# Optimization experiments

Measured on AMD Instinct MI355X. Metric: run time of the kernel, lower is better.

The kernel has to match this reference:

```python
import jax, jax.numpy as jnp
import numpy as np

H = 16       # num_attention_heads
D = 64       # head_dim
WIN = 256    # local attention window_size


def setup_inputs() -> dict:
    key = jax.random.key(0)
    ks = jax.random.split(key, 6)
    B, S, E = 2, 2048, 1024
    sc = 1.0 / np.sqrt(E)
    return {
        "hidden_states": jax.random.normal(ks[0], (B, S, E), jnp.float32),
        "Wq": jax.random.normal(ks[1], (E, E), jnp.float32) * sc,
        "Wk": jax.random.normal(ks[2], (E, E), jnp.float32) * sc,
        "Wv": jax.random.normal(ks[3], (E, E), jnp.float32) * sc,
        "Wo": jax.random.normal(ks[4], (E, E), jnp.float32) * sc,
        "bo": jnp.zeros((E,), jnp.float32),
    }


def reference(hidden_states, Wq, Wk, Wv, Wo, bo):
    B, S, E = hidden_states.shape
    # torch Linear: y = x @ W^T
    q = (hidden_states @ Wq.T).reshape(B, S, H, D).transpose(0, 2, 1, 3)  # [B,H,S,D]
    k = (hidden_states @ Wk.T).reshape(B, S, H, D).transpose(0, 2, 1, 3)
    v = (hidden_states @ Wv.T).reshape(B, S, H, D).transpose(0, 2, 1, 3)

    # Eager path: fp32 QK^T, NO 1/sqrt(d) scaling (faithful to source)
    scores = jnp.einsum("bhqd,bhkd->bhqk", q.astype(jnp.float32), k.astype(jnp.float32))

    i = jnp.arange(S)[:, None]
    j = jnp.arange(S)[None, :]
    band = (j <= i) & (j > i - WIN)  # [S,S]
    mask_value = jnp.finfo(scores.dtype).min
    scores = jnp.where(band[None, None], scores, mask_value)

    attn = jax.nn.softmax(scores, axis=-1).astype(v.dtype)  # dropout p=0 -> identity
    ctx = jnp.einsum("bhqk,bhkd->bhqd", attn, v)              # [B,H,S,D]
    ctx = ctx.transpose(0, 2, 1, 3).reshape(B, S, E)          # merge heads
    return ctx @ Wo.T + bo
```

## Files before the change

### kernel.cpp

```cpp
#include <hip/hip_runtime.h>


typedef __bf16 bf16x8 __attribute__((ext_vector_type(8)));
typedef short s16x8 __attribute__((ext_vector_type(8)));
typedef float f32x4 __attribute__((ext_vector_type(4)));
typedef unsigned short u16;

#define DEV __device__ __forceinline__

DEV u16 f2bf(float f) {
  unsigned u = __builtin_bit_cast(unsigned, f);
  u += 0x7FFFu + ((u >> 16) & 1u);
  return (u16)(u >> 16);
}
DEV float bf2f(u16 h) {
  unsigned u = ((unsigned)h) << 16;
  return __builtin_bit_cast(float, u);
}

#define MFMA16(a, b, c) __builtin_amdgcn_mfma_f32_16x16x32_bf16((a), (b), (c), 0, 0, 0)

template <bool LO>
__global__ __launch_bounds__(256) void cvt_split(const float* __restrict__ src,
                                                 u16* __restrict__ hi,
                                                 u16* __restrict__ lo, int n4) {
  for (int i = blockIdx.x * 256 + threadIdx.x; i < n4; i += gridDim.x * 256) {
    f32x4 v = ((const f32x4*)src)[i];
    unsigned long long ph = 0, pl = 0;
#pragma unroll
    for (int c = 0; c < 4; ++c) {
      u16 h = f2bf(v[c]);
      ph |= ((unsigned long long)h) << (16 * c);
      if (LO) {
        u16 l = f2bf(v[c] - bf2f(h));
        pl |= ((unsigned long long)l) << (16 * c);
      }
    }
    ((unsigned long long*)hi)[i] = ph;
    if (LO) ((unsigned long long*)lo)[i] = pl;
  }
}

template <int MODE>
__global__ __launch_bounds__(256) void gemm_kernel(
    const u16* __restrict__ Ah, const u16* __restrict__ Al,
    const u16* __restrict__ Bh, const u16* __restrict__ Bl,
    u16* __restrict__ O1, u16* __restrict__ O2,
    const float* __restrict__ bias, float* __restrict__ Of) {
  constexpr bool SPLIT = (MODE == 0);
  constexpr int NS = SPLIT ? 2 : 1;
  constexpr int BKP = 40;
  __shared__ u16 sA[NS][128][BKP];
  __shared__ u16 sB[NS][128][BKP];

  const int tid = threadIdx.x;
  const int lane = tid & 63, w = tid >> 6;
  const int lr = lane & 15, lg = lane >> 4;
  const int wr = w >> 1, wc = w & 1;
  const int m0 = blockIdx.y * 128, n0 = blockIdx.x * 128;

  f32x4 acc[4][4];
#pragma unroll
  for (int i = 0; i < 4; ++i)
#pragma unroll
    for (int j = 0; j < 4; ++j)
#pragma unroll
      for (int e = 0; e < 4; ++e) acc[i][j][e] = 0.f;

  for (int k0 = 0; k0 < 1024; k0 += 32) {
#pragma unroll
    for (int c = 0; c < 2; ++c) {
      int cid = c * 256 + tid;
      int row = cid >> 2, col8 = (cid & 3) * 8;
      size_t aoff = (size_t)(m0 + row) * 1024 + k0 + col8;
      size_t boff = (size_t)(n0 + row) * 1024 + k0 + col8;
      *(s16x8*)&sA[0][row][col8] = *(const s16x8*)&Ah[aoff];
      *(s16x8*)&sB[0][row][col8] = *(const s16x8*)&Bh[boff];
      if constexpr (SPLIT) {
        *(s16x8*)&sA[1][row][col8] = *(const s16x8*)&Al[aoff];
        *(s16x8*)&sB[1][row][col8] = *(const s16x8*)&Bl[boff];
      }
    }
    __syncthreads();

    bf16x8 fah[4], fbh[4], fal[4], fbl[4];
#pragma unroll
    for (int f = 0; f < 4; ++f) {
      fah[f] = *(const bf16x8*)&sA[0][wr * 64 + f * 16 + lr][lg * 8];
      fbh[f] = *(const bf16x8*)&sB[0][wc * 64 + f * 16 + lr][lg * 8];
      if constexpr (SPLIT) {
        fal[f] = *(const bf16x8*)&sA[1][wr * 64 + f * 16 + lr][lg * 8];
        fbl[f] = *(const bf16x8*)&sB[1][wc * 64 + f * 16 + lr][lg * 8];
      }
    }
#pragma unroll
    for (int i = 0; i < 4; ++i)
#pragma unroll
      for (int j = 0; j < 4; ++j) {
        acc[i][j] = MFMA16(fah[i], fbh[j], acc[i][j]);
        if constexpr (SPLIT) {
          acc[i][j] = MFMA16(fah[i], fbl[j], acc[i][j]);
          acc[i][j] = MFMA16(fal[i], fbh[j], acc[i][j]);
        }
      }
    __syncthreads();
  }

#pragma unroll
  for (int i = 0; i < 4; ++i)
#pragma unroll
    for (int j = 0; j < 4; ++j)
#pragma unroll
      for (int e = 0; e < 4; ++e) {
        float v = acc[i][j][e];
        int mm = m0 + wr * 64 + i * 16 + lg * 4 + e;
        int nn = n0 + wc * 64 + j * 16 + lr;
        if constexpr (MODE == 0) {
          int bb = mm >> 11, ss = mm & 2047, hh = nn >> 6, dd = nn & 63;
          size_t idx = ((size_t)(bb * 16 + hh) * 2048 + ss) * 64 + dd;
          u16 h = f2bf(v);
          O1[idx] = h;
          O2[idx] = f2bf(v - bf2f(h));
        } else if constexpr (MODE == 1) {
          int bb = mm >> 11, ss = mm & 2047, hh = nn >> 6, dd = nn & 63;
          size_t idx = ((size_t)(bb * 16 + hh) * 64 + dd) * 2048 + ss;
          O1[idx] = f2bf(v);
        } else {
          Of[(size_t)mm * 1024 + nn] = v + bias[nn];
        }
      }
}

__global__ __launch_bounds__(256) void attn_kernel(
    const u16* __restrict__ qh, const u16* __restrict__ ql,
    const u16* __restrict__ kh, const u16* __restrict__ kl,
    const u16* __restrict__ vT, u16* __restrict__ ctx) {
  const int qt = blockIdx.x, hd = blockIdx.y, b = blockIdx.z;
  const int q0 = qt * 64;
  const int bh = b * 16 + hd;
  const int tid = threadIdx.x;
  const int lane = tid & 63, w = tid >> 6;
  const int lr = lane & 15, lg = lane >> 4;

  __shared__ u16 sKh[64][72];
  __shared__ u16 sKl[64][72];
  __shared__ u16 sVT[64][72];
  __shared__ u16 sP[4][16][72];

  bf16x8 qfh[2], qfl[2];
  const size_t qbase = ((size_t)bh * 2048 + q0 + w * 16 + lr) * 64;
#pragma unroll
  for (int ks = 0; ks < 2; ++ks) {
    qfh[ks] = *(const bf16x8*)&qh[qbase + ks * 32 + lg * 8];
    qfl[ks] = *(const bf16x8*)&ql[qbase + ks * 32 + lg * 8];
  }

  float mrow[4], lrow[4];
  f32x4 cf[4];
#pragma unroll
  for (int e = 0; e < 4; ++e) { mrow[e] = -__builtin_inff(); lrow[e] = 0.f; }
#pragma unroll
  for (int nd = 0; nd < 4; ++nd)
#pragma unroll
    for (int e = 0; e < 4; ++e) cf[nd][e] = 0.f;

  const int t0 = (qt >= 4) ? qt - 4 : 0;
  for (int t = t0; t <= qt; ++t) {
    const int k0 = t * 64;
#pragma unroll
    for (int c = 0; c < 2; ++c) {
      int cid = c * 256 + tid;
      int row = cid >> 3, col8 = (cid & 7) * 8;
      size_t kidx = ((size_t)bh * 2048 + k0 + row) * 64 + col8;
      size_t vidx = ((size_t)bh * 64 + row) * 2048 + k0 + col8;
      *(s16x8*)&sKh[row][col8] = *(const s16x8*)&kh[kidx];
      *(s16x8*)&sKl[row][col8] = *(const s16x8*)&kl[kidx];
      *(s16x8*)&sVT[row][col8] = *(const s16x8*)&vT[vidx];
    }
    __syncthreads();

    f32x4 sc[4];
#pragma unroll
    for (int nf = 0; nf < 4; ++nf)
#pragma unroll
      for (int e = 0; e < 4; ++e) sc[nf][e] = 0.f;
#pragma unroll
    for (int ks = 0; ks < 2; ++ks)
#pragma unroll
      for (int nf = 0; nf < 4; ++nf) {
        bf16x8 kbh = *(const bf16x8*)&sKh[nf * 16 + lr][ks * 32 + lg * 8];
        bf16x8 kbl = *(const bf16x8*)&sKl[nf * 16 + lr][ks * 32 + lg * 8];
        sc[nf] = MFMA16(qfh[ks], kbh, sc[nf]);
        sc[nf] = MFMA16(qfh[ks], kbl, sc[nf]);
        sc[nf] = MFMA16(qfl[ks], kbh, sc[nf]);
      }

    const bool masked = (k0 < q0 - 192) || (k0 >= q0);
    if (masked) {
#pragma unroll
      for (int nf = 0; nf < 4; ++nf) {
        int key = k0 + nf * 16 + lr;
#pragma unroll
        for (int e = 0; e < 4; ++e) {
          int qi = q0 + w * 16 + lg * 4 + e;
          if (key > qi || key + 256 <= qi) sc[nf][e] = -__builtin_inff();
        }
      }
    }

    float rm[4];
#pragma unroll
    for (int e = 0; e < 4; ++e)
      rm[e] = fmaxf(fmaxf(sc[0][e], sc[1][e]), fmaxf(sc[2][e], sc[3][e]));
#pragma unroll
    for (int off = 1; off < 16; off <<= 1)
#pragma unroll
      for (int e = 0; e < 4; ++e) rm[e] = fmaxf(rm[e], __shfl_xor(rm[e], off));

    float alpha[4], mu[4];
#pragma unroll
    for (int e = 0; e < 4; ++e) {
      float mn = fmaxf(mrow[e], rm[e]);
      bool ninf = (mn == -__builtin_inff());
      mu[e] = ninf ? 0.f : mn;
      alpha[e] = ninf ? 1.f : __expf(mrow[e] - mn);
      mrow[e] = mn;
    }
    float p[4][4], rs[4];
#pragma unroll
    for (int nf = 0; nf < 4; ++nf)
#pragma unroll
      for (int e = 0; e < 4; ++e) p[nf][e] = __expf(sc[nf][e] - mu[e]);
#pragma unroll
    for (int e = 0; e < 4; ++e) rs[e] = p[0][e] + p[1][e] + p[2][e] + p[3][e];
#pragma unroll
    for (int off = 1; off < 16; off <<= 1)
#pragma unroll
      for (int e = 0; e < 4; ++e) rs[e] += __shfl_xor(rs[e], off);
#pragma unroll
    for (int e = 0; e < 4; ++e) lrow[e] = lrow[e] * alpha[e] + rs[e];
#pragma unroll
    for (int nd = 0; nd < 4; ++nd)
#pragma unroll
      for (int e = 0; e < 4; ++e) cf[nd][e] *= alpha[e];

#pragma unroll
    for (int nf = 0; nf < 4; ++nf)
#pragma unroll
      for (int e = 0; e < 4; ++e)
        sP[w][lg * 4 + e][nf * 16 + lr] = f2bf(p[nf][e]);

#pragma unroll
    for (int ks = 0; ks < 2; ++ks) {
      bf16x8 pa = *(const bf16x8*)&sP[w][lr][ks * 32 + lg * 8];
#pragma unroll
      for (int nd = 0; nd < 4; ++nd) {
        bf16x8 vb = *(const bf16x8*)&sVT[nd * 16 + lr][ks * 32 + lg * 8];
        cf[nd] = MFMA16(pa, vb, cf[nd]);
      }
    }
    __syncthreads();
  }

#pragma unroll
  for (int nd = 0; nd < 4; ++nd)
#pragma unroll
    for (int e = 0; e < 4; ++e) {
      float v = cf[nd][e] / lrow[e];
      size_t o = ((size_t)(b * 2048 + q0 + w * 16 + lg * 4 + e)) * 1024 +
                 hd * 64 + nd * 16 + lr;
      ctx[o] = f2bf(v);
    }
}

extern "C" void kernel_launch(void* const* d_in, const int* in_sizes, int n_in,
                              void* d_out, int out_size, void* d_ws, size_t ws_size,
                              hipStream_t stream) {
  (void)in_sizes; (void)n_in; (void)out_size; (void)ws_size;
  const float* x  = (const float*)d_in[0];
  const float* Wq = (const float*)d_in[1];
  const float* Wk = (const float*)d_in[2];
  const float* Wv = (const float*)d_in[3];
  const float* Wo = (const float*)d_in[4];
  const float* bo = (const float*)d_in[5];
  float* out = (float*)d_out;
  char* ws = (char*)d_ws;

  constexpr size_t TEN = 8388608;
  constexpr size_t WTEN = 2097152;
  u16* xh  = (u16*)(ws + 0 * TEN);
  u16* xl  = (u16*)(ws + 1 * TEN);
  u16* qh  = (u16*)(ws + 2 * TEN);
  u16* ql  = (u16*)(ws + 3 * TEN);
  u16* kh  = (u16*)(ws + 4 * TEN);
  u16* kl  = (u16*)(ws + 5 * TEN);
  u16* vT  = (u16*)(ws + 6 * TEN);
  u16* ctx = (u16*)(ws + 7 * TEN);
  char* wb = ws + 8 * TEN;
  u16* wqh = (u16*)(wb + 0 * WTEN);
  u16* wql = (u16*)(wb + 1 * WTEN);
  u16* wkh = (u16*)(wb + 2 * WTEN);
  u16* wkl = (u16*)(wb + 3 * WTEN);
  u16* wvh = (u16*)(wb + 4 * WTEN);
  u16* woh = (u16*)(wb + 5 * WTEN);

  cvt_split<true><<<1024, 256, 0, stream>>>(x, xh, xl, 4194304 / 4);
  cvt_split<true><<<256, 256, 0, stream>>>(Wq, wqh, wql, 1048576 / 4);
  cvt_split<true><<<256, 256, 0, stream>>>(Wk, wkh, wkl, 1048576 / 4);
  cvt_split<false><<<256, 256, 0, stream>>>(Wv, wvh, nullptr, 1048576 / 4);
  cvt_split<false><<<256, 256, 0, stream>>>(Wo, woh, nullptr, 1048576 / 4);

  dim3 gg(8, 32), bb(256);
  gemm_kernel<0><<<gg, bb, 0, stream>>>(xh, xl, wqh, wql, qh, ql, nullptr, nullptr);
  gemm_kernel<0><<<gg, bb, 0, stream>>>(xh, xl, wkh, wkl, kh, kl, nullptr, nullptr);
  gemm_kernel<1><<<gg, bb, 0, stream>>>(xh, nullptr, wvh, nullptr, vT, nullptr, nullptr, nullptr);
  attn_kernel<<<dim3(32, 16, 2), bb, 0, stream>>>(qh, ql, kh, kl, vT, ctx);
  gemm_kernel<2><<<gg, bb, 0, stream>>>(ctx, nullptr, woh, nullptr, nullptr, nullptr, bo, out);
}
```

Baseline: 280.4 us.

## Fuse conversions and QKV projections into single launches with direct-to-LDS loads

Merges the five fp32-to-bf16 conversion launches into one kernel and the three Q/K/V projection GEMMs into one grid of 24x32 blocks, where each block picks its hi/lo split mode and output layout from its column region. Tile staging now uses global_load_lds so data goes straight from global memory into LDS instead of through registers, and the LDS tile padding is removed. The aim is to cut launch overhead, fill the GPU better with a single larger grid, and reduce register pressure during staging. The unpadded LDS layout may cause bank conflicts on fragment reads, and the runtime branch on region adds some divergence-free control overhead.

Measured after the change: 309.1 us. +10.2%, slower.

```diff
diff --git a/kernel.cpp b/kernel.cpp
--- a/kernel.cpp
+++ b/kernel.cpp
@@ -5,6 +5,7 @@
 typedef short s16x8 __attribute__((ext_vector_type(8)));
 typedef float f32x4 __attribute__((ext_vector_type(4)));
 typedef unsigned short u16;
+typedef unsigned long long u64;
 
 #define DEV __device__ __forceinline__
 
@@ -20,44 +21,71 @@
 
 #define MFMA16(a, b, c) __builtin_amdgcn_mfma_f32_16x16x32_bf16((a), (b), (c), 0, 0, 0)
 
-template <bool LO>
-__global__ __launch_bounds__(256) void cvt_split(const float* __restrict__ src,
-                                                 u16* __restrict__ hi,
-                                                 u16* __restrict__ lo, int n4) {
-  for (int i = blockIdx.x * 256 + threadIdx.x; i < n4; i += gridDim.x * 256) {
-    f32x4 v = ((const f32x4*)src)[i];
-    unsigned long long ph = 0, pl = 0;
+DEV void gload16(const u16* g, u16* l) {
+  __builtin_amdgcn_global_load_lds(
+      (const __attribute__((address_space(1))) void*)(const void*)g,
+      (__attribute__((address_space(3))) void*)(void*)l, 16, 0, 0);
+}
+
+DEV void stage_tile(const u16* __restrict__ g, size_t stride, int r0, int k0,
+                    u16* lds, int w, int lane) {
+#pragma unroll
+  for (int c = 0; c < 2; ++c) {
+    int ch = c * 256 + (w << 6) + lane;
+    gload16(&g[(size_t)(r0 + (ch >> 2)) * stride + k0 + ((ch & 3) << 3)],
+            lds + (size_t)(c * 4 + w) * 512);
+  }
+}
+
+__global__ __launch_bounds__(256) void cvt_all(
+    const float* __restrict__ x, const float* __restrict__ Wq,
+    const float* __restrict__ Wk, const float* __restrict__ Wv,
+    const float* __restrict__ Wo, u16* __restrict__ xh, u16* __restrict__ xl,
+    u16* __restrict__ wh, u16* __restrict__ wl, u16* __restrict__ woh) {
+  for (int i = blockIdx.x * 256 + threadIdx.x; i < 2097152;
+       i += gridDim.x * 256) {
+    const float* src;
+    u16 *dh, *dl = nullptr;
+    int off;
+    bool sp;
+    if (i < 1048576) {
+      src = x; off = i; dh = xh; dl = xl; sp = true;
+    } else {
+      int j = i - 1048576;
+      int r = j >> 18;
+      off = j & 262143;
+      if (r == 0)      { src = Wq; dh = wh;           dl = wl;           sp = true; }
+      else if (r == 1) { src = Wk; dh = wh + 1048576; dl = wl + 1048576; sp = true; }
+      else if (r == 2) { src = Wv; dh = wh + 2097152; sp = false; }
+      else             { src = Wo; dh = woh;          sp = false; }
+    }
+    f32x4 v = ((const f32x4*)src)[off];
+    u64 ph = 0, pl = 0;
 #pragma unroll
     for (int c = 0; c < 4; ++c) {
       u16 h = f2bf(v[c]);
-      ph |= ((unsigned long long)h) << (16 * c);
-      if (LO) {
-        u16 l = f2bf(v[c] - bf2f(h));
-        pl |= ((unsigned long long)l) << (16 * c);
-      }
-    }
-    ((unsigned long long*)hi)[i] = ph;
-    if (LO) ((unsigned long long*)lo)[i] = pl;
-  }
-}
-
-template <int MODE>
-__global__ __launch_bounds__(256) void gemm_kernel(
-    const u16* __restrict__ Ah, const u16* __restrict__ Al,
-    const u16* __restrict__ Bh, const u16* __restrict__ Bl,
-    u16* __restrict__ O1, u16* __restrict__ O2,
-    const float* __restrict__ bias, float* __restrict__ Of) {
-  constexpr bool SPLIT = (MODE == 0);
-  constexpr int NS = SPLIT ? 2 : 1;
-  constexpr int BKP = 40;
-  __shared__ u16 sA[NS][128][BKP];
-  __shared__ u16 sB[NS][128][BKP];
-
-  const int tid = threadIdx.x;
-  const int lane = tid & 63, w = tid >> 6;
+      ph |= ((u64)h) << (16 * c);
+      u16 l = f2bf(v[c] - bf2f(h));
+      pl |= ((u64)l) << (16 * c);
+    }
+    ((u64*)dh)[off] = ph;
+    if (sp) ((u64*)dl)[off] = pl;
+  }
+}
+
+__global__ __launch_bounds__(256, 3) void qkv_gemm(
+    const u16* __restrict__ Xh, const u16* __restrict__ Xl,
+    const u16* __restrict__ Wh, const u16* __restrict__ Wl,
+    u16* __restrict__ qh, u16* __restrict__ ql, u16* __restrict__ kh,
+    u16* __restrict__ kl, u16* __restrict__ vT) {
+  __shared__ u16 sAh[128 * 32], sAl[128 * 32];
+  __shared__ u16 sBh[128 * 32], sBl[128 * 32];
+  const int tid = threadIdx.x, lane = tid & 63, w = tid >> 6;
   const int lr = lane & 15, lg = lane >> 4;
   const int wr = w >> 1, wc = w & 1;
   const int m0 = blockIdx.y * 128, n0 = blockIdx.x * 128;
+  const int region = n0 >> 10;
+  const bool split = region < 2;
 
   f32x4 acc[4][4];
 #pragma unroll
@@ -68,41 +96,41 @@
       for (int e = 0; e < 4; ++e) acc[i][j][e] = 0.f;
 
   for (int k0 = 0; k0 < 1024; k0 += 32) {
-#pragma unroll
-    for (int c = 0; c < 2; ++c) {
-      int cid = c * 256 + tid;
-      int row = cid >> 2, col8 = (cid & 3) * 8;
-      size_t aoff = (size_t)(m0 + row) * 1024 + k0 + col8;
-      size_t boff = (size_t)(n0 + row) * 1024 + k0 + col8;
-      *(s16x8*)&sA[0][row][col8] = *(const s16x8*)&Ah[aoff];
-      *(s16x8*)&sB[0][row][col8] = *(const s16x8*)&Bh[boff];
-      if constexpr (SPLIT) {
-        *(s16x8*)&sA[1][row][col8] = *(const s16x8*)&Al[aoff];
-        *(s16x8*)&sB[1][row][col8] = *(const s16x8*)&Bl[boff];
-      }
+    stage_tile(Xh, 1024, m0, k0, sAh, w, lane);
+    stage_tile(Wh, 1024, n0, k0, sBh, w, lane);
+    if (split) {
+      stage_tile(Xl, 1024, m0, k0, sAl, w, lane);
+      stage_tile(Wl, 1024, n0, k0, sBl, w, lane);
     }
     __syncthreads();
 
     bf16x8 fah[4], fbh[4], fal[4], fbl[4];
 #pragma unroll
     for (int f = 0; f < 4; ++f) {
-      fah[f] = *(const bf16x8*)&sA[0][wr * 64 + f * 16 + lr][lg * 8];
-      fbh[f] = *(const bf16x8*)&sB[0][wc * 64 + f * 16 + lr][lg * 8];
-      if constexpr (SPLIT) {
-        fal[f] = *(const bf16x8*)&sA[1][wr * 64 + f * 16 + lr][lg * 8];
-        fbl[f] = *(const bf16x8*)&sB[1][wc * 64 + f * 16 + lr][lg * 8];
-      }
-    }
-#pragma unroll
-    for (int i = 0; i < 4; ++i)
-#pragma unroll
-      for (int j = 0; j < 4; ++j) {
-        acc[i][j] = MFMA16(fah[i], fbh[j], acc[i][j]);
-        if constexpr (SPLIT) {
+      fah[f] = *(const bf16x8*)&sAh[(wr * 64 + f * 16 + lr) * 32 + lg * 8];
+      fbh[f] = *(const bf16x8*)&sBh[(wc * 64 + f * 16 + lr) * 32 + lg * 8];
+    }
+    if (split) {
+#pragma unroll
+      for (int f = 0; f < 4; ++f) {
+        fal[f] = *(const bf16x8*)&sAl[(wr * 64 + f * 16 + lr) * 32 + lg * 8];
+        fbl[f] = *(const bf16x8*)&sBl[(wc * 64 + f * 16 + lr) * 32 + lg * 8];
+      }
+#pragma unroll
+      for (int i = 0; i < 4; ++i)
+#pragma unroll
+        for (int j = 0; j < 4; ++j) {
+          acc[i][j] = MFMA16(fah[i], fbh[j], acc[i][j]);
           acc[i][j] = MFMA16(fah[i], fbl[j], acc[i][j]);
           acc[i][j] = MFMA16(fal[i], fbh[j], acc[i][j]);
         }
-      }
+    } else {
+#pragma unroll
+      for (int i = 0; i < 4; ++i)
+#pragma unroll
+        for (int j = 0; j < 4; ++j)
+          acc[i][j] = MFMA16(fah[i], fbh[j], acc[i][j]);
+    }
     __syncthreads();
   }
 
@@ -114,20 +142,67 @@
       for (int e = 0; e < 4; ++e) {
         float v = acc[i][j][e];
         int mm = m0 + wr * 64 + i * 16 + lg * 4 + e;
-        int nn = n0 + wc * 64 + j * 16 + lr;
-        if constexpr (MODE == 0) {
-          int bb = mm >> 11, ss = mm & 2047, hh = nn >> 6, dd = nn & 63;
+        int nl = (n0 & 1023) + wc * 64 + j * 16 + lr;
+        int bb = mm >> 11, ss = mm & 2047, hh = nl >> 6, dd = nl & 63;
+        if (region == 0) {
           size_t idx = ((size_t)(bb * 16 + hh) * 2048 + ss) * 64 + dd;
           u16 h = f2bf(v);
-          O1[idx] = h;
-          O2[idx] = f2bf(v - bf2f(h));
-        } else if constexpr (MODE == 1) {
-          int bb = mm >> 11, ss = mm & 2047, hh = nn >> 6, dd = nn & 63;
-          size_t idx = ((size_t)(bb * 16 + hh) * 64 + dd) * 2048 + ss;
-          O1[idx] = f2bf(v);
+          qh[idx] = h;
+          ql[idx] = f2bf(v - bf2f(h));
+        } else if (region == 1) {
+          size_t idx = ((size_t)(bb * 16 + hh) * 2048 + ss) * 64 + dd;
+          u16 h = f2bf(v);
+          kh[idx] = h;
+          kl[idx] = f2bf(v - bf2f(h));
         } else {
-          Of[(size_t)mm * 1024 + nn] = v + bias[nn];
+          vT[((size_t)(bb * 16 + hh) * 64 + dd) * 2048 + ss] = f2bf(v);
         }
+      }
+}
+
+__global__ __launch_bounds__(256) void out_gemm(const u16* __restrict__ ctx,
+                                                const u16* __restrict__ Wo,
+                                                const float* __restrict__ bias,
+                                                float* __restrict__ Of) {
+  __shared__ u16 sA[128 * 32], sB[128 * 32];
+  const int tid = threadIdx.x, lane = tid & 63, w = tid >> 6;
+  const int lr = lane & 15, lg = lane >> 4;
+  const int wr = w >> 1, wc = w & 1;
+  const int m0 = blockIdx.y * 128, n0 = blockIdx.x * 128;
+
+  f32x4 acc[4][4];
+#pragma unroll
+  for (int i = 0; i < 4; ++i)
+#pragma unroll
+    for (int j = 0; j < 4; ++j)
+#pragma unroll
+      for (int e = 0; e < 4; ++e) acc[i][j][e] = 0.f;
+
+  for (int k0 = 0; k0 < 1024; k0 += 32) {
+    stage_tile(ctx, 1024, m0, k0, sA, w, lane);
+    stage_tile(Wo, 1024, n0, k0, sB, w, lane);
+    __syncthreads();
+    bf16x8 fa[4], fb[4];
+#pragma unroll
+    for (int f = 0; f < 4; ++f) {
+      fa[f] = *(const bf16x8*)&sA[(wr * 64 + f * 16 + lr) * 32 + lg * 8];
+      fb[f] = *(const bf16x8*)&sB[(wc * 64 + f * 16 + lr) * 32 + lg * 8];
+    }
+#pragma unroll
+    for (int i = 0; i < 4; ++i)
+#pragma unroll
+      for (int j = 0; j < 4; ++j) acc[i][j] = MFMA16(fa[i], fb[j], acc[i][j]);
+    __syncthreads();
+  }
+#pragma unroll
+  for (int i = 0; i < 4; ++i)
+#pragma unroll
+    for (int j = 0; j < 4; ++j)
+#pragma unroll
+      for (int e = 0; e < 4; ++e) {
+        int mm = m0 + wr * 64 + i * 16 + lg * 4 + e;
+        int nn = n0 + wc * 64 + j * 16 + lr;
+        Of[(size_t)mm * 1024 + nn] = acc[i][j][e] + bias[nn];
       }
 }
 
@@ -286,34 +361,21 @@
   float* out = (float*)d_out;
   char* ws = (char*)d_ws;
 
-  constexpr size_t TEN = 8388608;
-  constexpr size_t WTEN = 2097152;
-  u16* xh  = (u16*)(ws + 0 * TEN);
-  u16* xl  = (u16*)(ws + 1 * TEN);
-  u16* qh  = (u16*)(ws + 2 * TEN);
-  u16* ql  = (u16*)(ws + 3 * TEN);
-  u16* kh  = (u16*)(ws + 4 * TEN);
-  u16* kl  = (u16*)(ws + 5 * TEN);
-  u16* vT  = (u16*)(ws + 6 * TEN);
-  u16* ctx = (u16*)(ws + 7 * TEN);
-  char* wb = ws + 8 * TEN;
-  u16* wqh = (u16*)(wb + 0 * WTEN);
-  u16* wql = (u16*)(wb + 1 * WTEN);
-  u16* wkh = (u16*)(wb + 2 * WTEN);
-  u16* wkl = (u16*)(wb + 3 * WTEN);
-  u16* wvh = (u16*)(wb + 4 * WTEN);
-  u16* woh = (u16*)(wb + 5 * WTEN);
-
-  cvt_split<true><<<1024, 256, 0, stream>>>(x, xh, xl, 4194304 / 4);
-  cvt_split<true><<<256, 256, 0, stream>>>(Wq, wqh, wql, 1048576 / 4);
-  cvt_split<true><<<256, 256, 0, stream>>>(Wk, wkh, wkl, 1048576 / 4);
-  cvt_split<false><<<256, 256, 0, stream>>>(Wv, wvh, nullptr, 1048576 / 4);
-  cvt_split<false><<<256, 256, 0, stream>>>(Wo, woh, nullptr, 1048576 / 4);
-
-  dim3 gg(8, 32), bb(256);
-  gemm_kernel<0><<<gg, bb, 0, stream>>>(xh, xl, wqh, wql, qh, ql, nullptr, nullptr);
-  gemm_kernel<0><<<gg, bb, 0, stream>>>(xh, xl, wkh, wkl, kh, kl, nullptr, nullptr);
-  gemm_kernel<1><<<gg, bb, 0, stream>>>(xh, nullptr, wvh, nullptr, vT, nullptr, nullptr, nullptr);
-  attn_kernel<<<dim3(32, 16, 2), bb, 0, stream>>>(qh, ql, kh, kl, vT, ctx);
-  gemm_kernel<2><<<gg, bb, 0, stream>>>(ctx, nullptr, woh, nullptr, nullptr, nullptr, bo, out);
-}
+  constexpr size_t MB = 1048576;
+  u16* xh  = (u16*)(ws + 0 * MB);
+  u16* xl  = (u16*)(ws + 8 * MB);
+  u16* qh  = (u16*)(ws + 16 * MB);
+  u16* ql  = (u16*)(ws + 24 * MB);
+  u16* kh  = (u16*)(ws + 32 * MB);
+  u16* kl  = (u16*)(ws + 40 * MB);
+  u16* vT  = (u16*)(ws + 48 * MB);
+  u16* ctx = (u16*)(ws + 56 * MB);
+  u16* wh  = (u16*)(ws + 64 * MB);
+  u16* wl  = (u16*)(ws + 70 * MB);
+  u16* woh = (u16*)(ws + 74 * MB);
+
+  cvt_all<<<2048, 256, 0, stream>>>(x, Wq, Wk, Wv, Wo, xh, xl, wh, wl, woh);
+  qkv_gemm<<<dim3(24, 32), 256, 0, stream>>>(xh, xl, wh, wl, qh, ql, kh, kl, vT);
+  attn_kernel<<<dim3(32, 16, 2), 256, 0, stream>>>(qh, ql, kh, kl, vT, ctx);
+  out_gemm<<<dim3(8, 32), 256, 0, stream>>>(ctx, woh, bo, out);
+}
```

## Fuse conversion kernels and store V row-major, transposing in attention LDS

Applied to the files above, without the earlier changes.

Replaces five separate fp32-to-bf16 split conversion launches with one combined kernel covering x and all four weights, which cuts launch overhead. The V projection now writes V in [B,H,S,D] layout instead of a transposed [B,H,D,S] layout, so the GEMM epilogue writes contiguous d indices. The attention kernel then transposes V into shared memory with scalar strided LDS stores, which may cause bank conflicts. The unified conversion loop also computes the low part for every element, even where it is not stored.

New measurement: 276.3 us. Within noise of the previous version (-1.5%).

```diff
diff --git a/kernel.cpp b/kernel.cpp
--- a/kernel.cpp
+++ b/kernel.cpp
@@ -5,6 +5,7 @@
 typedef short s16x8 __attribute__((ext_vector_type(8)));
 typedef float f32x4 __attribute__((ext_vector_type(4)));
 typedef unsigned short u16;
+typedef unsigned long long u64;
 
 #define DEV __device__ __forceinline__
 
@@ -20,24 +21,39 @@
 
 #define MFMA16(a, b, c) __builtin_amdgcn_mfma_f32_16x16x32_bf16((a), (b), (c), 0, 0, 0)
 
-template <bool LO>
-__global__ __launch_bounds__(256) void cvt_split(const float* __restrict__ src,
-                                                 u16* __restrict__ hi,
-                                                 u16* __restrict__ lo, int n4) {
-  for (int i = blockIdx.x * 256 + threadIdx.x; i < n4; i += gridDim.x * 256) {
-    f32x4 v = ((const f32x4*)src)[i];
-    unsigned long long ph = 0, pl = 0;
+__global__ __launch_bounds__(256) void cvt_all(
+    const float* __restrict__ x, const float* __restrict__ Wq,
+    const float* __restrict__ Wk, const float* __restrict__ Wv,
+    const float* __restrict__ Wo, u16* __restrict__ xh, u16* __restrict__ xl,
+    u16* __restrict__ wh, u16* __restrict__ wl, u16* __restrict__ woh) {
+  for (int i = blockIdx.x * 256 + threadIdx.x; i < 2097152;
+       i += gridDim.x * 256) {
+    const float* src;
+    u16 *dh, *dl = nullptr;
+    int off;
+    bool sp;
+    if (i < 1048576) {
+      src = x; off = i; dh = xh; dl = xl; sp = true;
+    } else {
+      int j = i - 1048576;
+      int r = j >> 18;
+      off = j & 262143;
+      if (r == 0)      { src = Wq; dh = wh;           dl = wl;           sp = true; }
+      else if (r == 1) { src = Wk; dh = wh + 1048576; dl = wl + 1048576; sp = true; }
+      else if (r == 2) { src = Wv; dh = wh + 2097152; sp = false; }
+      else             { src = Wo; dh = woh;          sp = false; }
+    }
+    f32x4 v = ((const f32x4*)src)[off];
+    u64 ph = 0, pl = 0;
 #pragma unroll
     for (int c = 0; c < 4; ++c) {
       u16 h = f2bf(v[c]);
-      ph |= ((unsigned long long)h) << (16 * c);
-      if (LO) {
-        u16 l = f2bf(v[c] - bf2f(h));
-        pl |= ((unsigned long long)l) << (16 * c);
-      }
-    }
-    ((unsigned long long*)hi)[i] = ph;
-    if (LO) ((unsigned long long*)lo)[i] = pl;
+      ph |= ((u64)h) << (16 * c);
+      u16 l = f2bf(v[c] - bf2f(h));
+      pl |= ((u64)l) << (16 * c);
+    }
+    ((u64*)dh)[off] = ph;
+    if (sp) ((u64*)dl)[off] = pl;
   }
 }
 
@@ -123,7 +139,7 @@
           O2[idx] = f2bf(v - bf2f(h));
         } else if constexpr (MODE == 1) {
           int bb = mm >> 11, ss = mm & 2047, hh = nn >> 6, dd = nn & 63;
-          size_t idx = ((size_t)(bb * 16 + hh) * 64 + dd) * 2048 + ss;
+          size_t idx = ((size_t)(bb * 16 + hh) * 2048 + ss) * 64 + dd;
           O1[idx] = f2bf(v);
         } else {
           Of[(size_t)mm * 1024 + nn] = v + bias[nn];
@@ -134,7 +150,7 @@
 __global__ __launch_bounds__(256) void attn_kernel(
     const u16* __restrict__ qh, const u16* __restrict__ ql,
     const u16* __restrict__ kh, const u16* __restrict__ kl,
-    const u16* __restrict__ vT, u16* __restrict__ ctx) {
+    const u16* __restrict__ vh, u16* __restrict__ ctx) {
   const int qt = blockIdx.x, hd = blockIdx.y, b = blockIdx.z;
   const int q0 = qt * 64;
   const int bh = b * 16 + hd;
@@ -172,10 +188,12 @@
       int cid = c * 256 + tid;
       int row = cid >> 3, col8 = (cid & 7) * 8;
       size_t kidx = ((size_t)bh * 2048 + k0 + row) * 64 + col8;
-      size_t vidx = ((size_t)bh * 64 + row) * 2048 + k0 + col8;
       *(s16x8*)&sKh[row][col8] = *(const s16x8*)&kh[kidx];
       *(s16x8*)&sKl[row][col8] = *(const s16x8*)&kl[kidx];
-      *(s16x8*)&sVT[row][col8] = *(const s16x8*)&vT[vidx];
+      s16x8 vv = *(const s16x8*)&vh[kidx];
+#pragma unroll
+      for (int j = 0; j < 8; ++j)
+        sVT[col8 + j][row] = (u16)vv[j];
     }
     __syncthreads();
 
@@ -286,34 +304,28 @@
   float* out = (float*)d_out;
   char* ws = (char*)d_ws;
 
-  constexpr size_t TEN = 8388608;
-  constexpr size_t WTEN = 2097152;
-  u16* xh  = (u16*)(ws + 0 * TEN);
-  u16* xl  = (u16*)(ws + 1 * TEN);
-  u16* qh  = (u16*)(ws + 2 * TEN);
-  u16* ql  = (u16*)(ws + 3 * TEN);
-  u16* kh  = (u16*)(ws + 4 * TEN);
-  u16* kl  = (u16*)(ws + 5 * TEN);
-  u16* vT  = (u16*)(ws + 6 * TEN);
-  u16* ctx = (u16*)(ws + 7 * TEN);
-  char* wb = ws + 8 * TEN;
-  u16* wqh = (u16*)(wb + 0 * WTEN);
-  u16* wql = (u16*)(wb + 1 * WTEN);
-  u16* wkh = (u16*)(wb + 2 * WTEN);
-  u16* wkl = (u16*)(wb + 3 * WTEN);
-  u16* wvh = (u16*)(wb + 4 * WTEN);
-  u16* woh = (u16*)(wb + 5 * WTEN);
-
-  cvt_split<true><<<1024, 256, 0, stream>>>(x, xh, xl, 4194304 / 4);
-  cvt_split<true><<<256, 256, 0, stream>>>(Wq, wqh, wql, 1048576 / 4);
-  cvt_split<true><<<256, 256, 0, stream>>>(Wk, wkh, wkl, 1048576 / 4);
-  cvt_split<false><<<256, 256, 0, stream>>>(Wv, wvh, nullptr, 1048576 / 4);
-  cvt_split<false><<<256, 256, 0, stream>>>(Wo, woh, nullptr, 1048576 / 4);
+  constexpr size_t MB = 1048576;
+  u16* xh  = (u16*)(ws + 0 * MB);
+  u16* xl  = (u16*)(ws + 8 * MB);
+  u16* qh  = (u16*)(ws + 16 * MB);
+  u16* ql  = (u16*)(ws + 24 * MB);
+  u16* kh  = (u16*)(ws + 32 * MB);
+  u16* kl  = (u16*)(ws + 40 * MB);
+  u16* vh  = (u16*)(ws + 48 * MB);
+  u16* ctx = (u16*)(ws + 56 * MB);
+  u16* wh  = (u16*)(ws + 64 * MB);
+  u16* wl  = (u16*)(ws + 70 * MB);
+  u16* woh = (u16*)(ws + 74 * MB);
+
+  cvt_all<<<2048, 256, 0, stream>>>(x, Wq, Wk, Wv, Wo, xh, xl, wh, wl, woh);
 
   dim3 gg(8, 32), bb(256);
-  gemm_kernel<0><<<gg, bb, 0, stream>>>(xh, xl, wqh, wql, qh, ql, nullptr, nullptr);
-  gemm_kernel<0><<<gg, bb, 0, stream>>>(xh, xl, wkh, wkl, kh, kl, nullptr, nullptr);
-  gemm_kernel<1><<<gg, bb, 0, stream>>>(xh, nullptr, wvh, nullptr, vT, nullptr, nullptr, nullptr);
-  attn_kernel<<<dim3(32, 16, 2), bb, 0, stream>>>(qh, ql, kh, kl, vT, ctx);
-  gemm_kernel<2><<<gg, bb, 0, stream>>>(ctx, nullptr, woh, nullptr, nullptr, nullptr, bo, out);
-}
+  gemm_kernel<0><<<gg, bb, 0, stream>>>(xh, xl, wh, wl, qh, ql, nullptr, nullptr);
+  gemm_kernel<0><<<gg, bb, 0, stream>>>(xh, xl, wh + 1048576, wl + 1048576,
+                                        kh, kl, nullptr, nullptr);
+  gemm_kernel<1><<<gg, bb, 0, stream>>>(xh, nullptr, wh + 2097152, nullptr,
+                                        vh, nullptr, nullptr, nullptr);
+  attn_kernel<<<dim3(32, 16, 2), bb, 0, stream>>>(qh, ql, kh, kl, vh, ctx);
+  gemm_kernel<2><<<gg, bb, 0, stream>>>(ctx, nullptr, woh, nullptr,
+                                        nullptr, nullptr, bo, out);
+}
```
